# Kernel optimization log

Hardware: AMD Instinct MI355X
Metric: run time of the kernel (lower is better)

The kernel has to match this reference:

```python
import jax, jax.numpy as jnp
import numpy as np

B = 1024        # number of graphs
MAXLEN = 64     # max nodes per graph (pad_sequence length)
E = 256         # hidden_size
H = 8           # num_heads
HD = E // H     # head dim
NEG = -1e9


def setup_inputs() -> dict:
    key = jax.random.key(0)
    k0, k1, k2 = jax.random.split(key, 3)
    lens = np.tile(np.array([32, 48, 64, 40], dtype=np.int64), B // 4)  # sum = 47104
    batch_indices = jnp.asarray(np.repeat(np.arange(B, dtype=np.int64), lens))
    N = int(lens.sum())
    node_features = jax.random.normal(k0, (N, E), dtype=jnp.float32)
    in_proj_w = jax.random.normal(k1, (3 * E, E), dtype=jnp.float32) * (1.0 / np.sqrt(E))
    in_proj_b = jnp.zeros((3 * E,), dtype=jnp.float32)
    out_proj_w = jax.random.normal(k2, (E, E), dtype=jnp.float32) * (1.0 / np.sqrt(E))
    out_proj_b = jnp.zeros((E,), dtype=jnp.float32)
    return {"node_features": node_features, "batch_indices": batch_indices,
            "in_proj_w": in_proj_w, "in_proj_b": in_proj_b,
            "out_proj_w": out_proj_w, "out_proj_b": out_proj_b}


def _pad_ragged(node_features, batch_indices):
    # counts per graph, start offset of each graph, position of each node in its graph
    N = node_features.shape[0]
    counts = jax.ops.segment_sum(jnp.ones((N,), jnp.int32), batch_indices, num_segments=B)
    starts = jnp.cumsum(counts) - counts
    pos = jnp.arange(N) - starts[batch_indices]
    padded = jnp.zeros((B, MAXLEN, E), node_features.dtype).at[batch_indices, pos].set(node_features)
    key_pad = jnp.arange(MAXLEN)[None, :] >= counts[:, None]  # [B, L] True = padding
    return padded, key_pad


def reference(node_features, batch_indices, in_proj_w, in_proj_b, out_proj_w, out_proj_b):
    padded, key_pad = _pad_ragged(node_features, batch_indices)   # [B,L,E], [B,L]
    qkv = padded @ in_proj_w.T + in_proj_b                        # [B,L,3E]
    q, k, v = jnp.split(qkv, 3, axis=-1)
    q = q.reshape(B, MAXLEN, H, HD)
    k = k.reshape(B, MAXLEN, H, HD)
    v = v.reshape(B, MAXLEN, H, HD)
    scores = jnp.einsum('blhd,bmhd->bhlm', q, k) / jnp.sqrt(jnp.float32(HD))
    scores = jnp.where(key_pad[:, None, None, :], NEG, scores)    # mask padded keys
    attn = jax.nn.softmax(scores, axis=-1)                        # [B,H,L,L]
    ctx = jnp.einsum('bhlm,bmhd->blhd', attn, v).reshape(B, MAXLEN, E)
    out = ctx @ out_proj_w.T + out_proj_b                         # [B,L,E]
    out = jnp.transpose(out, (1, 0, 2))                           # [L,B,E] seq-first like torch
    weights = attn.mean(axis=1)                                   # [B,L,L] head-averaged
    return out, weights
```

## Files before the change

kernel.cpp:

```cpp
#include <hip/hip_runtime.h>

typedef unsigned short u16;
typedef short bf16x8 __attribute__((ext_vector_type(8)));
typedef float f32x4 __attribute__((ext_vector_type(4)));

#define MFMA16(a, b, c) __builtin_amdgcn_mfma_f32_16x16x32_bf16((a), (b), (c), 0, 0, 0)

static __device__ __forceinline__ u16 f2bf(float f) {
    union { float f; unsigned int u; } v; v.f = f;
    unsigned int u = v.u;
    u += 0x7fffu + ((u >> 16) & 1u);
    return (u16)(u >> 16);
}

__global__ void prep_kernel(const int* __restrict__ bidx, int N,
                            const float* __restrict__ w_in, const float* __restrict__ w_out,
                            int* __restrict__ starts, int* __restrict__ counts,
                            u16* __restrict__ w_in_bf, u16* __restrict__ w_out_bf) {
    int tid = blockIdx.x * blockDim.x + threadIdx.x;
    if (tid < 1024) {
        int lo = 0, hi = N;
        while (lo < hi) { int mid = (lo + hi) >> 1; if (bidx[mid] < tid) lo = mid + 1; else hi = mid; }
        int s0 = lo;
        lo = 0; hi = N;
        int v1 = tid + 1;
        while (lo < hi) { int mid = (lo + hi) >> 1; if (bidx[mid] < v1) lo = mid + 1; else hi = mid; }
        starts[tid] = s0;
        counts[tid] = lo - s0;
    }
    {
        float4 v = ((const float4*)w_in)[tid];
        ushort4 o; o.x = f2bf(v.x); o.y = f2bf(v.y); o.z = f2bf(v.z); o.w = f2bf(v.w);
        ((ushort4*)w_in_bf)[tid] = o;
    }
    if (tid < 16384) {
        float4 v = ((const float4*)w_out)[tid];
        ushort4 o; o.x = f2bf(v.x); o.y = f2bf(v.y); o.z = f2bf(v.z); o.w = f2bf(v.w);
        ((ushort4*)w_out_bf)[tid] = o;
    }
}

__global__ __launch_bounds__(512, 4) void gat_kernel(
    const float* __restrict__ X, const float* __restrict__ bias_in,
    const float* __restrict__ bias_out,
    const int* __restrict__ starts, const int* __restrict__ counts,
    const u16* __restrict__ w_in_bf, const u16* __restrict__ w_out_bf,
    float* __restrict__ out, float* __restrict__ wout) {

    __shared__ u16 qg[64][72];
    __shared__ u16 kg[64][72];
    __shared__ u16 vt[64][72];
    __shared__ u16 p_s[8][16][72];
    __shared__ u16 cs[64][256];

    const int b = blockIdx.x;
    const int tid = threadIdx.x;
    const int w = tid >> 6;
    const int lane = tid & 63;
    const int n = lane & 15;
    const int quad = lane >> 4;
    const int s = starts[b];
    const int c = counts[b];

    const int wh = w >> 2;
    const int wj = w & 3;
    const int hh = w & 1;
    const int rt = w >> 1;
    const int m0 = rt * 16;

    bf16x8 afr[2][8];
    #pragma unroll
    for (int st2 = 0; st2 < 2; ++st2) {
        int row = wh * 32 + st2 * 16 + n;
        bool ok = row < c;
        const float* src = X + (long)(s + row) * 256 + quad * 8;
        #pragma unroll
        for (int ks = 0; ks < 8; ++ks) {
            float4 v0 = make_float4(0.f, 0.f, 0.f, 0.f);
            float4 v1 = make_float4(0.f, 0.f, 0.f, 0.f);
            if (ok) {
                v0 = *(const float4*)(src + ks * 32);
                v1 = *(const float4*)(src + ks * 32 + 4);
            }
            bf16x8 a;
            a[0] = (short)f2bf(v0.x); a[1] = (short)f2bf(v0.y);
            a[2] = (short)f2bf(v0.z); a[3] = (short)f2bf(v0.w);
            a[4] = (short)f2bf(v1.x); a[5] = (short)f2bf(v1.y);
            a[6] = (short)f2bf(v1.z); a[7] = (short)f2bf(v1.w);
            afr[st2][ks] = a;
        }
    }

    const float scale = 0.17677669529663687f;
    float wacc[4][4];
    #pragma unroll
    for (int t = 0; t < 4; ++t)
        #pragma unroll
        for (int r = 0; r < 4; ++r) wacc[t][r] = 0.f;

    #pragma unroll 1
    for (int g = 0; g < 4; ++g) {
        #pragma unroll 1
        for (int i = 0; i < 3; ++i) {
            const int wrow = i * 256 + g * 64 + wj * 16 + n;
            const u16* wr = w_in_bf + wrow * 256 + quad * 8;
            const float bias = bias_in[wrow];

            f32x4 acc[2];
            acc[0] = (f32x4){0.f, 0.f, 0.f, 0.f};
            acc[1] = (f32x4){0.f, 0.f, 0.f, 0.f};
            #pragma unroll
            for (int kh = 0; kh < 2; ++kh) {
                bf16x8 bfr[4];
                #pragma unroll
                for (int k4 = 0; k4 < 4; ++k4) bfr[k4] = *(const bf16x8*)(wr + (kh * 4 + k4) * 32);
                #pragma unroll
                for (int k4 = 0; k4 < 4; ++k4) {
                    acc[0] = MFMA16(afr[0][kh * 4 + k4], bfr[k4], acc[0]);
                    acc[1] = MFMA16(afr[1][kh * 4 + k4], bfr[k4], acc[1]);
                }
            }

            #pragma unroll
            for (int st2 = 0; st2 < 2; ++st2) {
                const int st = 2 * wh + st2;
                if (i == 2) {
                    ushort4 pk;
                    pk.x = f2bf(acc[st2][0] + bias); pk.y = f2bf(acc[st2][1] + bias);
                    pk.z = f2bf(acc[st2][2] + bias); pk.w = f2bf(acc[st2][3] + bias);
                    *(ushort4*)&vt[wj * 16 + n][st * 16 + quad * 4] = pk;
                } else {
                    u16 (*dst)[72] = i ? kg : qg;
                    #pragma unroll
                    for (int r = 0; r < 4; ++r)
                        dst[st * 16 + quad * 4 + r][wj * 16 + n] = f2bf(acc[st2][r] + bias);
                }
            }
        }
        __syncthreads();

        {
            const int h = g * 2 + hh;
            bf16x8 aq = *(const bf16x8*)&qg[m0 + n][hh * 32 + quad * 8];
            f32x4 sc[4];
            #pragma unroll
            for (int t = 0; t < 4; ++t) {
                bf16x8 bk = *(const bf16x8*)&kg[t * 16 + n][hh * 32 + quad * 8];
                f32x4 z = (f32x4){0.f, 0.f, 0.f, 0.f};
                sc[t] = MFMA16(bk, aq, z);
            }
            float pv[4][4];
            float mx = -1e30f;
            #pragma unroll
            for (int t = 0; t < 4; ++t)
                #pragma unroll
                for (int r = 0; r < 4; ++r) {
                    float sv = ((t * 16 + quad * 4 + r) < c) ? sc[t][r] * scale : -1e30f;
                    pv[t][r] = sv;
                    mx = fmaxf(mx, sv);
                }
            mx = fmaxf(mx, __shfl_xor(mx, 16, 64));
            mx = fmaxf(mx, __shfl_xor(mx, 32, 64));
            float sm = 0.f;
            #pragma unroll
            for (int t = 0; t < 4; ++t)
                #pragma unroll
                for (int r = 0; r < 4; ++r) {
                    float e = ((t * 16 + quad * 4 + r) < c) ? __expf(pv[t][r] - mx) : 0.f;
                    pv[t][r] = e; sm += e;
                }
            sm += __shfl_xor(sm, 16, 64);
            sm += __shfl_xor(sm, 32, 64);
            float invs = 1.f / sm;
            #pragma unroll
            for (int t = 0; t < 4; ++t)
                #pragma unroll
                for (int r = 0; r < 4; ++r) {
                    pv[t][r] *= invs;
                    wacc[t][r] += pv[t][r] * 0.125f;
                }
            #pragma unroll
            for (int t = 0; t < 4; ++t) {
                ushort4 pk;
                pk.x = f2bf(pv[t][0]); pk.y = f2bf(pv[t][1]);
                pk.z = f2bf(pv[t][2]); pk.w = f2bf(pv[t][3]);
                *(ushort4*)&p_s[w][n][t * 16 + quad * 4] = pk;
            }
            #pragma unroll
            for (int nt = 0; nt < 2; ++nt) {
                f32x4 acc = (f32x4){0.f, 0.f, 0.f, 0.f};
                #pragma unroll
                for (int k2 = 0; k2 < 2; ++k2) {
                    bf16x8 ap = *(const bf16x8*)&p_s[w][n][k2 * 32 + quad * 8];
                    bf16x8 bv = *(const bf16x8*)&vt[hh * 32 + nt * 16 + n][k2 * 32 + quad * 8];
                    acc = MFMA16(ap, bv, acc);
                }
                #pragma unroll
                for (int r = 0; r < 4; ++r)
                    cs[m0 + quad * 4 + r][h * 32 + nt * 16 + n] = f2bf(acc[r]);
            }
        }
        __syncthreads();
    }

    {
        float* pw = (float*)&p_s[w & ~1][0][0];
        if (hh == 0) {
            #pragma unroll
            for (int t = 0; t < 4; ++t) {
                float4 f4 = make_float4(wacc[t][0], wacc[t][1], wacc[t][2], wacc[t][3]);
                *(float4*)&pw[n * 72 + t * 16 + quad * 4] = f4;
            }
        }
        __syncthreads();
        if (hh == 1) {
            #pragma unroll
            for (int t = 0; t < 4; ++t) {
                float4 f4 = *(const float4*)&pw[n * 72 + t * 16 + quad * 4];
                float4 o;
                o.x = wacc[t][0] + f4.x; o.y = wacc[t][1] + f4.y;
                o.z = wacc[t][2] + f4.z; o.w = wacc[t][3] + f4.w;
                *(float4*)&wout[b * 4096 + (m0 + n) * 64 + t * 16 + quad * 4] = o;
            }
        }
    }

    {
        const int sp = w & 1;
        const int cq = w >> 1;
        bf16x8 actx[2][8];
        #pragma unroll
        for (int st2 = 0; st2 < 2; ++st2)
            #pragma unroll
            for (int ks = 0; ks < 8; ++ks)
                actx[st2][ks] = *(const bf16x8*)&cs[(2 * sp + st2) * 16 + n][ks * 32 + quad * 8];

        #pragma unroll 2
        for (int ci = 0; ci < 4; ++ci) {
            const int ct = 4 * cq + ci;
            const u16* wr = w_out_bf + (ct * 16 + n) * 256 + quad * 8;
            f32x4 acc[2];
            acc[0] = (f32x4){0.f, 0.f, 0.f, 0.f};
            acc[1] = (f32x4){0.f, 0.f, 0.f, 0.f};
            #pragma unroll
            for (int kh = 0; kh < 2; ++kh) {
                bf16x8 bfr[4];
                #pragma unroll
                for (int k4 = 0; k4 < 4; ++k4) bfr[k4] = *(const bf16x8*)(wr + (kh * 4 + k4) * 32);
                #pragma unroll
                for (int k4 = 0; k4 < 4; ++k4) {
                    acc[0] = MFMA16(actx[0][kh * 4 + k4], bfr[k4], acc[0]);
                    acc[1] = MFMA16(actx[1][kh * 4 + k4], bfr[k4], acc[1]);
                }
            }
            float bias = bias_out[ct * 16 + n];
            #pragma unroll
            for (int st2 = 0; st2 < 2; ++st2) {
                const int orow = (2 * sp + st2) * 16 + quad * 4;
                #pragma unroll
                for (int r = 0; r < 4; ++r)
                    out[(orow + r) * 262144 + b * 256 + ct * 16 + n] = acc[st2][r] + bias;
            }
        }
    }
}

extern "C" void kernel_launch(void* const* d_in, const int* in_sizes, int n_in,
                              void* d_out, int out_size, void* d_ws, size_t ws_size,
                              hipStream_t stream) {
    const float* X     = (const float*)d_in[0];
    const int*   bidx  = (const int*)d_in[1];
    const float* w_in  = (const float*)d_in[2];
    const float* b_in  = (const float*)d_in[3];
    const float* w_out = (const float*)d_in[4];
    const float* b_out = (const float*)d_in[5];
    const int N = in_sizes[1];

    float* out  = (float*)d_out;
    float* wout = out + 64 * 1024 * 256;

    int* starts   = (int*)d_ws;
    int* counts   = starts + 1024;
    u16* w_in_bf  = (u16*)(counts + 1024);
    u16* w_out_bf = w_in_bf + 196608;

    hipLaunchKernelGGL(prep_kernel, dim3(192), dim3(256), 0, stream,
                       bidx, N, w_in, w_out, starts, counts, w_in_bf, w_out_bf);
    hipLaunchKernelGGL(gat_kernel, dim3(1024), dim3(512), 0, stream,
                       X, b_in, b_out, starts, counts, w_in_bf, w_out_bf, out, wout);
}
```

Baseline: 288.0 us.

## Pre-convert node features to bf16 and reload A fragments per group

The prep kernel now converts all node features to bf16 into workspace, when the workspace is large enough. The attention kernel reloads the A-operand fragments from this bf16 copy inside each head-group iteration instead of keeping 16 fragments live across the whole kernel, which lowers register pressure. The shared context buffer row is also padded to 264 to avoid LDS bank conflicts. The cost is an extra full pass over X in a small 192-block prep kernel and four reloads of X per block.

```diff
diff --git a/kernel.cpp b/kernel.cpp
--- a/kernel.cpp
+++ b/kernel.cpp
@@ -14,9 +14,11 @@
 }
 
 __global__ void prep_kernel(const int* __restrict__ bidx, int N,
+                            const float* __restrict__ X,
                             const float* __restrict__ w_in, const float* __restrict__ w_out,
                             int* __restrict__ starts, int* __restrict__ counts,
-                            u16* __restrict__ w_in_bf, u16* __restrict__ w_out_bf) {
+                            u16* __restrict__ w_in_bf, u16* __restrict__ w_out_bf,
+                            u16* __restrict__ xbf) {
     int tid = blockIdx.x * blockDim.x + threadIdx.x;
     if (tid < 1024) {
         int lo = 0, hi = N;
@@ -38,11 +40,24 @@
         ushort4 o; o.x = f2bf(v.x); o.y = f2bf(v.y); o.z = f2bf(v.z); o.w = f2bf(v.w);
         ((ushort4*)w_out_bf)[tid] = o;
     }
+    if (xbf) {
+        int total = N * 32;
+        for (int i = tid; i < total; i += 49152) {
+            float4 v0 = ((const float4*)X)[2 * i];
+            float4 v1 = ((const float4*)X)[2 * i + 1];
+            bf16x8 o;
+            o[0] = (short)f2bf(v0.x); o[1] = (short)f2bf(v0.y);
+            o[2] = (short)f2bf(v0.z); o[3] = (short)f2bf(v0.w);
+            o[4] = (short)f2bf(v1.x); o[5] = (short)f2bf(v1.y);
+            o[6] = (short)f2bf(v1.z); o[7] = (short)f2bf(v1.w);
+            ((bf16x8*)xbf)[i] = o;
+        }
+    }
 }
 
 __global__ __launch_bounds__(512, 4) void gat_kernel(
-    const float* __restrict__ X, const float* __restrict__ bias_in,
-    const float* __restrict__ bias_out,
+    const float* __restrict__ X, const u16* __restrict__ xbf,
+    const float* __restrict__ bias_in, const float* __restrict__ bias_out,
     const int* __restrict__ starts, const int* __restrict__ counts,
     const u16* __restrict__ w_in_bf, const u16* __restrict__ w_out_bf,
     float* __restrict__ out, float* __restrict__ wout) {
@@ -51,7 +66,7 @@
     __shared__ u16 kg[64][72];
     __shared__ u16 vt[64][72];
     __shared__ u16 p_s[8][16][72];
-    __shared__ u16 cs[64][256];
+    __shared__ u16 cs[64][264];
 
     const int b = blockIdx.x;
     const int tid = threadIdx.x;
@@ -68,29 +83,6 @@
     const int rt = w >> 1;
     const int m0 = rt * 16;
 
-    bf16x8 afr[2][8];
-    #pragma unroll
-    for (int st2 = 0; st2 < 2; ++st2) {
-        int row = wh * 32 + st2 * 16 + n;
-        bool ok = row < c;
-        const float* src = X + (long)(s + row) * 256 + quad * 8;
-        #pragma unroll
-        for (int ks = 0; ks < 8; ++ks) {
-            float4 v0 = make_float4(0.f, 0.f, 0.f, 0.f);
-            float4 v1 = make_float4(0.f, 0.f, 0.f, 0.f);
-            if (ok) {
-                v0 = *(const float4*)(src + ks * 32);
-                v1 = *(const float4*)(src + ks * 32 + 4);
-            }
-            bf16x8 a;
-            a[0] = (short)f2bf(v0.x); a[1] = (short)f2bf(v0.y);
-            a[2] = (short)f2bf(v0.z); a[3] = (short)f2bf(v0.w);
-            a[4] = (short)f2bf(v1.x); a[5] = (short)f2bf(v1.y);
-            a[6] = (short)f2bf(v1.z); a[7] = (short)f2bf(v1.w);
-            afr[st2][ks] = a;
-        }
-    }
-
     const float scale = 0.17677669529663687f;
     float wacc[4][4];
     #pragma unroll
@@ -100,6 +92,39 @@
 
     #pragma unroll 1
     for (int g = 0; g < 4; ++g) {
+        bf16x8 afr[2][8];
+        #pragma unroll
+        for (int st2 = 0; st2 < 2; ++st2) {
+            const int row = wh * 32 + st2 * 16 + n;
+            const bool ok = row < c;
+            if (xbf) {
+                const u16* src = xbf + (long)(s + row) * 256 + quad * 8;
+                #pragma unroll
+                for (int ks = 0; ks < 8; ++ks) {
+                    bf16x8 a = (bf16x8){0, 0, 0, 0, 0, 0, 0, 0};
+                    if (ok) a = *(const bf16x8*)(src + ks * 32);
+                    afr[st2][ks] = a;
+                }
+            } else {
+                const float* src = X + (long)(s + row) * 256 + quad * 8;
+                #pragma unroll
+                for (int ks = 0; ks < 8; ++ks) {
+                    float4 v0 = make_float4(0.f, 0.f, 0.f, 0.f);
+                    float4 v1 = make_float4(0.f, 0.f, 0.f, 0.f);
+                    if (ok) {
+                        v0 = *(const float4*)(src + ks * 32);
+                        v1 = *(const float4*)(src + ks * 32 + 4);
+                    }
+                    bf16x8 a;
+                    a[0] = (short)f2bf(v0.x); a[1] = (short)f2bf(v0.y);
+                    a[2] = (short)f2bf(v0.z); a[3] = (short)f2bf(v0.w);
+                    a[4] = (short)f2bf(v1.x); a[5] = (short)f2bf(v1.y);
+                    a[6] = (short)f2bf(v1.z); a[7] = (short)f2bf(v1.w);
+                    afr[st2][ks] = a;
+                }
+            }
+        }
+
         #pragma unroll 1
         for (int i = 0; i < 3; ++i) {
             const int wrow = i * 256 + g * 64 + wj * 16 + n;
@@ -283,9 +308,14 @@
     int* counts   = starts + 1024;
     u16* w_in_bf  = (u16*)(counts + 1024);
     u16* w_out_bf = w_in_bf + 196608;
+    u16* xbf      = w_out_bf + 65536;
+
+    const size_t base_need = 2048ull * 4 + 196608ull * 2 + 65536ull * 2;
+    const size_t xbf_bytes = (size_t)N * 256 * 2;
+    if (ws_size < base_need + xbf_bytes) xbf = nullptr;
 
     hipLaunchKernelGGL(prep_kernel, dim3(192), dim3(256), 0, stream,
-                       bidx, N, w_in, w_out, starts, counts, w_in_bf, w_out_bf);
+                       bidx, N, X, w_in, w_out, starts, counts, w_in_bf, w_out_bf, xbf);
     hipLaunchKernelGGL(gat_kernel, dim3(1024), dim3(512), 0, stream,
-                       X, b_in, b_out, starts, counts, w_in_bf, w_out_bf, out, wout);
+                       X, xbf, b_in, b_out, starts, counts, w_in_bf, w_out_bf, out, wout);
 }
```

Result: slower. 370.0 us (+28.5%).
